# Kernel optimization log

Hardware: AMD Instinct MI355X
Metric: run time of the kernel (lower is better)

## Reference

```python
import jax, jax.numpy as jnp
import numpy as np

N_NODES = 10000
N_EDGES = 160000
F_IN = 128
F_OUT = 128
BATCH = 8


def setup_inputs() -> dict:
    key = jax.random.key(0)
    k1, k2, k3, k4 = jax.random.split(key, 4)
    scale = 1.0 / np.sqrt(F_IN)
    x = jax.random.normal(k1, (BATCH, N_NODES, F_IN), dtype=jnp.float32)
    W_l = jax.random.normal(k2, (F_OUT, F_IN), dtype=jnp.float32) * scale
    b_l = jnp.zeros((F_OUT,), dtype=jnp.float32)
    W_r = jax.random.normal(k3, (F_OUT, F_IN), dtype=jnp.float32) * scale
    edge_index = jax.random.randint(k4, (2, N_EDGES), 0, N_NODES, dtype=jnp.int64)
    return {"x": x, "W_l": W_l, "b_l": b_l, "W_r": W_r, "edge_index": edge_index}


def reference(x, W_l, b_l, W_r, edge_index):
    # SAGEConv (PyG, mean aggr): out_i = W_l @ mean_{j->i} x_j + b_l + W_r @ x_i
    src = edge_index[0]  # message source nodes
    dst = edge_index[1]  # message target nodes
    deg = jax.ops.segment_sum(jnp.ones((src.shape[0],), x.dtype), dst,
                              num_segments=N_NODES)  # [N]
    deg = jnp.maximum(deg, 1.0)[:, None]  # avoid div-by-zero

    def agg_one(xs):  # xs: [N, F]
        msgs = xs[src]  # [E, F] gather
        return jax.ops.segment_sum(msgs, dst, num_segments=N_NODES) / deg

    mean_nbr = jax.vmap(agg_one)(x)  # [B, N, F]
    out = jnp.einsum('bnf,of->bno', mean_nbr, W_l) + b_l \
        + jnp.einsum('bnf,of->bno', x, W_r)
    return out
```

## Files before the change

kernel.cpp:

```cpp
#include <hip/hip_runtime.h>
#include <hip/hip_bf16.h>

#define N_NODES 10000
#define N_EDGES 160000
#define F_IN    128
#define F_OUT   128
#define BATCH   8
#define NROWS   (BATCH * N_NODES)

#define WS_FLAG_OFF   0
#define WS_WT_OFF     256
#define WS_DEG_OFF    131328
#define WS_ROW_OFF    171328
#define WS_CUR_OFF    211332
#define WS_COL_OFF    251332
#define WS_TOTAL      891332

#define WS2_FLAG  0
#define WS2_WT    256
#define WS2_DEG   65792
#define WS2_ROW   105792
#define WS2_CUR   145796
#define WS2_COL   185796
#define WS2_XH    825856
#define WS2_Z     21305856
#define WS2_TOTAL 62265856

typedef __attribute__((ext_vector_type(8))) short short8;
typedef __attribute__((ext_vector_type(4))) float floatx4;

__device__ __forceinline__ int edge_val(const void* ei, int idx, int i64) {
    if (i64) return (int)((const long long*)ei)[idx];
    return ((const int*)ei)[idx];
}

__global__ void detect_i64_kernel(const void* ei, int* flag) {
    __shared__ int any_nonzero;
    if (threadIdx.x == 0) any_nonzero = 0;
    __syncthreads();
    int v = ((const int*)ei)[2 * threadIdx.x + 1];
    if (v != 0) atomicOr(&any_nonzero, 1);
    __syncthreads();
    if (threadIdx.x == 0) *flag = (any_nonzero == 0) ? 1 : 0;
}

__global__ void hist_kernel(const void* ei, const int* __restrict__ flag,
                            int* __restrict__ deg) {
    int e = blockIdx.x * 256 + threadIdx.x;
    if (e >= N_EDGES) return;
    int i64 = *flag;
    int d = edge_val(ei, N_EDGES + e, i64);
    atomicAdd(&deg[d], 1);
}

__global__ __launch_bounds__(1024)
void scan_kernel(const int* __restrict__ deg, int* __restrict__ row_start) {
    __shared__ int sd[1024];
    const int CH = (N_NODES + 1023) / 1024;
    int t = threadIdx.x;
    int beg = t * CH;
    int end = min(N_NODES, beg + CH);
    int s = 0;
    for (int i = beg; i < end; i++) s += deg[i];
    sd[t] = s;
    __syncthreads();
    for (int off = 1; off < 1024; off <<= 1) {
        int v = (t >= off) ? sd[t - off] : 0;
        __syncthreads();
        sd[t] += v;
        __syncthreads();
    }
    int run = sd[t] - s;
    for (int i = beg; i < end; i++) { row_start[i] = run; run += deg[i]; }
    if (t == 1023) row_start[N_NODES] = sd[1023];
}

__global__ void scatter_kernel(const void* ei, const int* __restrict__ flag,
                               const int* __restrict__ row_start,
                               int* __restrict__ cursor, int* __restrict__ col) {
    int e = blockIdx.x * 256 + threadIdx.x;
    if (e >= N_EDGES) return;
    int i64 = *flag;
    int s = edge_val(ei, e, i64);
    int d = edge_val(ei, N_EDGES + e, i64);
    int pos = atomicAdd(&cursor[d], 1);
    col[row_start[d] + pos] = s;
}


__device__ __forceinline__ unsigned short f2bf(float v) {
    __hip_bfloat16 h = __float2bfloat16(v);
    return *(unsigned short*)&h;
}

__device__ __forceinline__ uint2 pack4(float4 v) {
    uint2 r;
    r.x = (unsigned)f2bf(v.x) | ((unsigned)f2bf(v.y) << 16);
    r.y = (unsigned)f2bf(v.z) | ((unsigned)f2bf(v.w) << 16);
    return r;
}

__device__ __forceinline__ void acc4(float4& a, uint2 p) {
    a.x += __uint_as_float(p.x << 16);
    a.y += __uint_as_float(p.x & 0xffff0000u);
    a.z += __uint_as_float(p.y << 16);
    a.w += __uint_as_float(p.y & 0xffff0000u);
}

__global__ void make_wt_bf16(const float* __restrict__ Wl,
                             const float* __restrict__ Wr,
                             unsigned short* __restrict__ Wt) {
    int idx = blockIdx.x * 256 + threadIdx.x;
    int o = idx >> 8;
    int k = idx & 255;
    float v = (k < F_IN) ? Wl[o * F_IN + k] : Wr[o * F_IN + (k - F_IN)];
    Wt[idx] = f2bf(v);
}

__global__ __launch_bounds__(256)
void convert_kernel(const float* __restrict__ x,
                    uint2* __restrict__ xh2, uint2* __restrict__ z2) {
    int t = blockIdx.x * 256 + threadIdx.x;
    float4 v = ((const float4*)x)[t];
    uint2 p = pack4(v);
    xh2[t] = p;
    int row = t >> 5, c = t & 31;
    z2[(size_t)row * 64 + 32 + c] = p;
}

__global__ __launch_bounds__(256)
void gather_bf16_kernel(const uint2* __restrict__ xh2,
                        const int* __restrict__ row_start,
                        const int* __restrict__ col,
                        uint2* __restrict__ z2) {
    __shared__ int nbr[1024];
    const int n = blockIdx.x;
    const int t = threadIdx.x;
    const int b = t >> 5;
    const int c = t & 31;

    const int beg = row_start[n];
    const int end = row_start[n + 1];
    const int d   = end - beg;
    const int cnt = min(d, 1024);

    for (int i = t; i < cnt; i += 256) nbr[i] = col[beg + i];
    __syncthreads();

    const size_t bbase = (size_t)b * N_NODES;

    float4 s0 = make_float4(0,0,0,0), s1 = s0, s2 = s0, s3 = s0;
    int i = 0;
    for (; i + 4 <= cnt; i += 4) {
        int n0 = nbr[i], n1 = nbr[i+1], n2 = nbr[i+2], n3 = nbr[i+3];
        uint2 v0 = xh2[(bbase + n0) * 32 + c];
        uint2 v1 = xh2[(bbase + n1) * 32 + c];
        uint2 v2 = xh2[(bbase + n2) * 32 + c];
        uint2 v3 = xh2[(bbase + n3) * 32 + c];
        acc4(s0, v0); acc4(s1, v1); acc4(s2, v2); acc4(s3, v3);
    }
    for (; i < cnt; i++) {
        uint2 v = xh2[(bbase + nbr[i]) * 32 + c];
        acc4(s0, v);
    }
    for (int j = 1024; j < d; j++) {
        uint2 v = xh2[(bbase + col[beg + j]) * 32 + c];
        acc4(s0, v);
    }
    s0.x += s1.x + s2.x + s3.x; s0.y += s1.y + s2.y + s3.y;
    s0.z += s1.z + s2.z + s3.z; s0.w += s1.w + s2.w + s3.w;
    const float inv = 1.0f / (float)max(d, 1);
    float4 m = make_float4(s0.x*inv, s0.y*inv, s0.z*inv, s0.w*inv);
    z2[((bbase + n)) * 64 + c] = pack4(m);
}

__global__ __launch_bounds__(256)
void gemm_bf16_kernel(const unsigned short* __restrict__ z,
                      const unsigned short* __restrict__ Wt,
                      const float* __restrict__ bl,
                      float* __restrict__ out) {
    __shared__ unsigned short A[64 * 256];

    const int tid = threadIdx.x;
    const int m0 = blockIdx.x * 64;

    #pragma unroll
    for (int it = 0; it < 8; ++it) {
        int byte = it * 4096 + tid * 16;
        int r = byte >> 9;
        int cch = (byte >> 4) & 31;
        uint4 v = *(const uint4*)(z + (size_t)(m0 + r) * 256 + cch * 8);
        int dch = cch ^ (r & 7);
        *(uint4*)((char*)A + r * 512 + dch * 16) = v;
    }
    __syncthreads();

    const int w  = tid >> 6;
    const int l  = tid & 63;
    const int lr = l & 15;
    const int kg = l >> 4;

    floatx4 acc[8];
    #pragma unroll
    for (int j = 0; j < 8; ++j) acc[j] = (floatx4){0.f, 0.f, 0.f, 0.f};

    #pragma unroll
    for (int ks = 0; ks < 8; ++ks) {
        const int r = w * 16 + lr;
        const int cch = ks * 4 + kg;
        short8 af = *(const short8*)((const char*)A + r * 512 + ((cch ^ (r & 7)) * 16));
        #pragma unroll
        for (int jt = 0; jt < 8; ++jt) {
            short8 bf = *(const short8*)(Wt + (size_t)(jt * 16 + lr) * 256 + ks * 32 + kg * 8);
            acc[jt] = __builtin_amdgcn_mfma_f32_16x16x32_bf16(af, bf, acc[jt], 0, 0, 0);
        }
    }

    #pragma unroll
    for (int jt = 0; jt < 8; ++jt) {
        const int colo = jt * 16 + lr;
        const float bias = bl[colo];
        const int rbase = m0 + w * 16 + kg * 4;
        #pragma unroll
        for (int q = 0; q < 4; ++q) {
            out[(size_t)(rbase + q) * F_OUT + colo] = acc[jt][q] + bias;
        }
    }
}


__global__ void transpose_w_kernel(const float* __restrict__ Wl,
                                   const float* __restrict__ Wr,
                                   float* __restrict__ Wt) {
    int idx = blockIdx.x * 256 + threadIdx.x;
    int f = idx >> 7;
    int o = idx & 127;
    float v = (f < F_IN) ? Wl[o * F_IN + f] : Wr[o * F_IN + (f - F_IN)];
    Wt[f * F_OUT + o] = v;
}

__global__ __launch_bounds__(256)
void sage_fused_kernel(const float* __restrict__ x,
                       const float* __restrict__ bl,
                       const float* __restrict__ Wt,
                       const int* __restrict__ row_start,
                       const int* __restrict__ col,
                       float* __restrict__ out) {
    __shared__ float in_lds[BATCH][2 * F_IN];

    const int n = blockIdx.x;
    const int t = threadIdx.x;
    const int b = t >> 5;
    const int c = t & 31;

    const int beg = row_start[n];
    const int end = row_start[n + 1];

    const float* xb = x + (size_t)b * N_NODES * F_IN;

    float4 acc = make_float4(0.f, 0.f, 0.f, 0.f);
    for (int i = beg; i < end; i++) {
        int s = col[i];
        const float4 v = *(const float4*)(xb + (size_t)s * F_IN + c * 4);
        acc.x += v.x; acc.y += v.y; acc.z += v.z; acc.w += v.w;
    }
    const float inv = 1.0f / (float)max(end - beg, 1);
    const float4 self = *(const float4*)(xb + (size_t)n * F_IN + c * 4);

    *(float4*)&in_lds[b][c * 4] =
        make_float4(acc.x * inv, acc.y * inv, acc.z * inv, acc.w * inv);
    *(float4*)&in_lds[b][F_IN + c * 4] = self;
    __syncthreads();

    float4 oacc = *(const float4*)(bl + c * 4);
    #pragma unroll 8
    for (int f4 = 0; f4 < 64; f4++) {
        const float4 inq = *(const float4*)&in_lds[b][f4 * 4];
        const float4 w0 = *(const float4*)(Wt + (f4 * 4 + 0) * F_OUT + c * 4);
        const float4 w1 = *(const float4*)(Wt + (f4 * 4 + 1) * F_OUT + c * 4);
        const float4 w2 = *(const float4*)(Wt + (f4 * 4 + 2) * F_OUT + c * 4);
        const float4 w3 = *(const float4*)(Wt + (f4 * 4 + 3) * F_OUT + c * 4);
        oacc.x += inq.x * w0.x; oacc.y += inq.x * w0.y; oacc.z += inq.x * w0.z; oacc.w += inq.x * w0.w;
        oacc.x += inq.y * w1.x; oacc.y += inq.y * w1.y; oacc.z += inq.y * w1.z; oacc.w += inq.y * w1.w;
        oacc.x += inq.z * w2.x; oacc.y += inq.z * w2.y; oacc.z += inq.z * w2.z; oacc.w += inq.z * w2.w;
        oacc.x += inq.w * w3.x; oacc.y += inq.w * w3.y; oacc.z += inq.w * w3.z; oacc.w += inq.w * w3.w;
    }

    *(float4*)(out + ((size_t)b * N_NODES + n) * F_OUT + c * 4) = oacc;
}

extern "C" void kernel_launch(void* const* d_in, const int* in_sizes, int n_in,
                              void* d_out, int out_size, void* d_ws, size_t ws_size,
                              hipStream_t stream) {
    const float* x  = (const float*)d_in[0];
    const float* Wl = (const float*)d_in[1];
    const float* bl = (const float*)d_in[2];
    const float* Wr = (const float*)d_in[3];
    const void*  ei = d_in[4];
    float* out = (float*)d_out;
    char* ws = (char*)d_ws;

    if (ws_size >= (size_t)WS2_TOTAL + 1024) {
        int*            flag = (int*)(ws + WS2_FLAG);
        unsigned short* Wt   = (unsigned short*)(ws + WS2_WT);
        int*            deg  = (int*)(ws + WS2_DEG);
        int*            rowp = (int*)(ws + WS2_ROW);
        int*            cur  = (int*)(ws + WS2_CUR);
        int*            col  = (int*)(ws + WS2_COL);
        uint2*          xh2  = (uint2*)(ws + WS2_XH);
        uint2*          z2   = (uint2*)(ws + WS2_Z);

        hipMemsetAsync(ws + WS2_DEG, 0, WS2_COL - WS2_DEG, stream);
        detect_i64_kernel<<<1, 256, 0, stream>>>(ei, flag);
        make_wt_bf16<<<128, 256, 0, stream>>>(Wl, Wr, Wt);
        hist_kernel<<<(N_EDGES + 255) / 256, 256, 0, stream>>>(ei, flag, deg);
        scan_kernel<<<1, 1024, 0, stream>>>(deg, rowp);
        scatter_kernel<<<(N_EDGES + 255) / 256, 256, 0, stream>>>(ei, flag, rowp, cur, col);
        convert_kernel<<<(NROWS * 32) / 256, 256, 0, stream>>>(x, xh2, z2);
        gather_bf16_kernel<<<N_NODES, 256, 0, stream>>>(xh2, rowp, col, z2);
        gemm_bf16_kernel<<<NROWS / 64, 256, 0, stream>>>(
            (const unsigned short*)z2, Wt, bl, out);
    } else {
        int*   flag      = (int*)(ws + WS_FLAG_OFF);
        float* Wt        = (float*)(ws + WS_WT_OFF);
        int*   deg       = (int*)(ws + WS_DEG_OFF);
        int*   row_start = (int*)(ws + WS_ROW_OFF);
        int*   cursor    = (int*)(ws + WS_CUR_OFF);
        int*   col       = (int*)(ws + WS_COL_OFF);

        hipMemsetAsync(d_ws, 0, WS_TOTAL, stream);
        detect_i64_kernel<<<1, 256, 0, stream>>>(ei, flag);
        transpose_w_kernel<<<(256 * 128) / 256, 256, 0, stream>>>(Wl, Wr, Wt);
        hist_kernel<<<(N_EDGES + 255) / 256, 256, 0, stream>>>(ei, flag, deg);
        scan_kernel<<<1, 1024, 0, stream>>>(deg, row_start);
        scatter_kernel<<<(N_EDGES + 255) / 256, 256, 0, stream>>>(ei, flag, row_start, cursor, col);
        sage_fused_kernel<<<N_NODES, 256, 0, stream>>>(x, bl, Wt, row_start, col, out);
    }
}
```

Before: 221.3 us.

## Fuse neighbor gather and bf16 MFMA GEMM into one kernel per 8-node tile

Merges the separate gather and GEMM kernels into one kernel. Each block aggregates 8 nodes across all 8 batches straight into a swizzled shared-memory A tile, then runs the MFMA GEMM and writes output rows mapped back to batch/node. This drops the 41MB intermediate z buffer write and re-read and one launch, and it lowers the workspace requirement. In exchange the grid shrinks to 1250 blocks that each do serial gather work over 8 nodes. The shared-memory staging of neighbor indices is also removed, so col is read directly from global memory.

After: 230.6 us. +4.2%, slower.

```diff
diff --git a/kernel.cpp b/kernel.cpp
--- a/kernel.cpp
+++ b/kernel.cpp
@@ -7,6 +7,7 @@
 #define F_OUT   128
 #define BATCH   8
 #define NROWS   (BATCH * N_NODES)
+#define NT      8
 
 #define WS_FLAG_OFF   0
 #define WS_WT_OFF     256
@@ -23,8 +24,7 @@
 #define WS2_CUR   145796
 #define WS2_COL   185796
 #define WS2_XH    825856
-#define WS2_Z     21305856
-#define WS2_TOTAL 62265856
+#define WS2_NEED  21305856
 
 typedef __attribute__((ext_vector_type(8))) short short8;
 typedef __attribute__((ext_vector_type(4))) float floatx4;
@@ -118,85 +118,63 @@
 }
 
 __global__ __launch_bounds__(256)
-void convert_kernel(const float* __restrict__ x,
-                    uint2* __restrict__ xh2, uint2* __restrict__ z2) {
+void convert_kernel(const float* __restrict__ x, uint2* __restrict__ xh2) {
     int t = blockIdx.x * 256 + threadIdx.x;
     float4 v = ((const float4*)x)[t];
-    uint2 p = pack4(v);
-    xh2[t] = p;
-    int row = t >> 5, c = t & 31;
-    z2[(size_t)row * 64 + 32 + c] = p;
+    xh2[t] = pack4(v);
 }
 
 __global__ __launch_bounds__(256)
-void gather_bf16_kernel(const uint2* __restrict__ xh2,
-                        const int* __restrict__ row_start,
-                        const int* __restrict__ col,
-                        uint2* __restrict__ z2) {
-    __shared__ int nbr[1024];
-    const int n = blockIdx.x;
-    const int t = threadIdx.x;
-    const int b = t >> 5;
-    const int c = t & 31;
-
-    const int beg = row_start[n];
-    const int end = row_start[n + 1];
-    const int d   = end - beg;
-    const int cnt = min(d, 1024);
-
-    for (int i = t; i < cnt; i += 256) nbr[i] = col[beg + i];
-    __syncthreads();
+void sage_fused_mfma(const uint2* __restrict__ xh2,
+                     const int* __restrict__ row_start,
+                     const int* __restrict__ col,
+                     const unsigned short* __restrict__ Wt,
+                     const float* __restrict__ bl,
+                     float* __restrict__ out) {
+    __shared__ unsigned short Z[64 * 256];
+
+    const int n0 = blockIdx.x * NT;
+    const int t  = threadIdx.x;
+    const int b  = t >> 5;
+    const int c  = t & 31;
 
     const size_t bbase = (size_t)b * N_NODES;
 
-    float4 s0 = make_float4(0,0,0,0), s1 = s0, s2 = s0, s3 = s0;
-    int i = 0;
-    for (; i + 4 <= cnt; i += 4) {
-        int n0 = nbr[i], n1 = nbr[i+1], n2 = nbr[i+2], n3 = nbr[i+3];
-        uint2 v0 = xh2[(bbase + n0) * 32 + c];
-        uint2 v1 = xh2[(bbase + n1) * 32 + c];
-        uint2 v2 = xh2[(bbase + n2) * 32 + c];
-        uint2 v3 = xh2[(bbase + n3) * 32 + c];
-        acc4(s0, v0); acc4(s1, v1); acc4(s2, v2); acc4(s3, v3);
-    }
-    for (; i < cnt; i++) {
-        uint2 v = xh2[(bbase + nbr[i]) * 32 + c];
-        acc4(s0, v);
-    }
-    for (int j = 1024; j < d; j++) {
-        uint2 v = xh2[(bbase + col[beg + j]) * 32 + c];
-        acc4(s0, v);
-    }
-    s0.x += s1.x + s2.x + s3.x; s0.y += s1.y + s2.y + s3.y;
-    s0.z += s1.z + s2.z + s3.z; s0.w += s1.w + s2.w + s3.w;
-    const float inv = 1.0f / (float)max(d, 1);
-    float4 m = make_float4(s0.x*inv, s0.y*inv, s0.z*inv, s0.w*inv);
-    z2[((bbase + n)) * 64 + c] = pack4(m);
-}
-
-__global__ __launch_bounds__(256)
-void gemm_bf16_kernel(const unsigned short* __restrict__ z,
-                      const unsigned short* __restrict__ Wt,
-                      const float* __restrict__ bl,
-                      float* __restrict__ out) {
-    __shared__ unsigned short A[64 * 256];
-
-    const int tid = threadIdx.x;
-    const int m0 = blockIdx.x * 64;
-
-    #pragma unroll
-    for (int it = 0; it < 8; ++it) {
-        int byte = it * 4096 + tid * 16;
-        int r = byte >> 9;
-        int cch = (byte >> 4) & 31;
-        uint4 v = *(const uint4*)(z + (size_t)(m0 + r) * 256 + cch * 8);
-        int dch = cch ^ (r & 7);
-        *(uint4*)((char*)A + r * 512 + dch * 16) = v;
-    }
-    __syncthreads();
-
-    const int w  = tid >> 6;
-    const int l  = tid & 63;
+    #pragma unroll 2
+    for (int ni = 0; ni < NT; ++ni) {
+        const int n   = n0 + ni;
+        const int beg = row_start[n];
+        const int end = row_start[n + 1];
+        const int d   = end - beg;
+
+        float4 s0 = make_float4(0.f,0.f,0.f,0.f), s1 = s0, s2 = s0, s3 = s0;
+        int i = beg;
+        for (; i + 4 <= end; i += 4) {
+            int m0 = col[i], m1 = col[i+1], m2 = col[i+2], m3 = col[i+3];
+            acc4(s0, xh2[(bbase + m0) * 32 + c]);
+            acc4(s1, xh2[(bbase + m1) * 32 + c]);
+            acc4(s2, xh2[(bbase + m2) * 32 + c]);
+            acc4(s3, xh2[(bbase + m3) * 32 + c]);
+        }
+        for (; i < end; ++i) acc4(s0, xh2[(bbase + col[i]) * 32 + c]);
+
+        s0.x += s1.x + s2.x + s3.x; s0.y += s1.y + s2.y + s3.y;
+        s0.z += s1.z + s2.z + s3.z; s0.w += s1.w + s2.w + s3.w;
+        const float inv = 1.0f / (float)max(d, 1);
+        uint2 mp = pack4(make_float4(s0.x*inv, s0.y*inv, s0.z*inv, s0.w*inv));
+        uint2 sp = xh2[(bbase + n) * 32 + c];
+
+        const int r   = b * 8 + ni;
+        const int sub = (c & 1) * 8;
+        const int cc0 = c >> 1;
+        const int cc1 = 16 + (c >> 1);
+        *(uint2*)((char*)Z + r * 512 + ((cc0 ^ (r & 7)) * 16) + sub) = mp;
+        *(uint2*)((char*)Z + r * 512 + ((cc1 ^ (r & 7)) * 16) + sub) = sp;
+    }
+    __syncthreads();
+
+    const int w  = t >> 6;
+    const int l  = t & 63;
     const int lr = l & 15;
     const int kg = l >> 4;
 
@@ -206,9 +184,9 @@
 
     #pragma unroll
     for (int ks = 0; ks < 8; ++ks) {
-        const int r = w * 16 + lr;
+        const int r   = w * 16 + lr;
         const int cch = ks * 4 + kg;
-        short8 af = *(const short8*)((const char*)A + r * 512 + ((cch ^ (r & 7)) * 16));
+        short8 af = *(const short8*)((const char*)Z + r * 512 + ((cch ^ (r & 7)) * 16));
         #pragma unroll
         for (int jt = 0; jt < 8; ++jt) {
             short8 bf = *(const short8*)(Wt + (size_t)(jt * 16 + lr) * 256 + ks * 32 + kg * 8);
@@ -220,10 +198,12 @@
     for (int jt = 0; jt < 8; ++jt) {
         const int colo = jt * 16 + lr;
         const float bias = bl[colo];
-        const int rbase = m0 + w * 16 + kg * 4;
+        const int rt = w * 16 + kg * 4;
         #pragma unroll
         for (int q = 0; q < 4; ++q) {
-            out[(size_t)(rbase + q) * F_OUT + colo] = acc[jt][q] + bias;
+            const int r = rt + q;
+            const int row = (r >> 3) * N_NODES + n0 + (r & 7);
+            out[(size_t)row * F_OUT + colo] = acc[jt][q] + bias;
         }
     }
 }
@@ -300,7 +280,7 @@
     float* out = (float*)d_out;
     char* ws = (char*)d_ws;
 
-    if (ws_size >= (size_t)WS2_TOTAL + 1024) {
+    if (ws_size >= (size_t)WS2_NEED + 1024) {
         int*            flag = (int*)(ws + WS2_FLAG);
         unsigned short* Wt   = (unsigned short*)(ws + WS2_WT);
         int*            deg  = (int*)(ws + WS2_DEG);
@@ -308,7 +288,6 @@
         int*            cur  = (int*)(ws + WS2_CUR);
         int*            col  = (int*)(ws + WS2_COL);
         uint2*          xh2  = (uint2*)(ws + WS2_XH);
-        uint2*          z2   = (uint2*)(ws + WS2_Z);
 
         hipMemsetAsync(ws + WS2_DEG, 0, WS2_COL - WS2_DEG, stream);
         detect_i64_kernel<<<1, 256, 0, stream>>>(ei, flag);
@@ -316,10 +295,8 @@
         hist_kernel<<<(N_EDGES + 255) / 256, 256, 0, stream>>>(ei, flag, deg);
         scan_kernel<<<1, 1024, 0, stream>>>(deg, rowp);
         scatter_kernel<<<(N_EDGES + 255) / 256, 256, 0, stream>>>(ei, flag, rowp, cur, col);
-        convert_kernel<<<(NROWS * 32) / 256, 256, 0, stream>>>(x, xh2, z2);
-        gather_bf16_kernel<<<N_NODES, 256, 0, stream>>>(xh2, rowp, col, z2);
-        gemm_bf16_kernel<<<NROWS / 64, 256, 0, stream>>>(
-            (const unsigned short*)z2, Wt, bl, out);
+        convert_kernel<<<(NROWS * 32) / 256, 256, 0, stream>>>(x, xh2);
+        sage_fused_mfma<<<N_NODES / NT, 256, 0, stream>>>(xh2, rowp, col, Wt, bl, out);
     } else {
         int*   flag      = (int*)(ws + WS_FLAG_OFF);
         float* Wt        = (float*)(ws + WS_WT_OFF);
```
